# Kernel optimization log

Hardware: AMD Instinct MI355X
Metric: run time of the kernel (lower is better)

Reference implementation:

```python
import jax, jax.numpy as jnp
import numpy as np

B, S, D, H, DK, DV = 4, 1024, 1024, 16, 64, 64
HALF = D // 2            # 512
DKH = DK // 2            # per-head half q/k dim = 32
DVH = DV // 2            # per-head half v dim = 32


def setup_inputs() -> dict:
    key = jax.random.key(0)
    ks = jax.random.split(key, 12)
    f = lambda k, sh: jax.random.normal(k, sh, dtype=jnp.float32)
    inp = {
        "input_Q": f(ks[0], (B, S, D)),
        "input_K": f(ks[1], (B, S, D)),
        "input_V": f(ks[2], (B, S, D)),
    }
    # causal mask (True = masked), matching attn_mask() helper for non-pad tokens
    causal = jnp.triu(jnp.ones((S, S), dtype=bool), k=1)
    inp["attn_mask"] = jnp.broadcast_to(causal, (B, S, S))
    scale = 0.02
    # projections: [in=HALF, out=DK*H//2=HALF] stored as (in, out) for x @ W
    for i, n in enumerate(["WQ1", "WK1", "WV1", "WQ2", "WK2", "WV2"]):
        inp[n] = f(ks[3 + i], (HALF, DK * H // 2)) * scale
    inp["Wfc1"] = f(ks[9], (H * DV // 2, HALF)) * scale
    inp["Wfc2"] = f(ks[10], (H * DV // 2, HALF)) * scale
    inp["ln_g"] = jnp.ones((HALF,), dtype=jnp.float32)
    inp["ln_b"] = jnp.zeros((HALF,), dtype=jnp.float32)
    return inp


def _layernorm(x, g, b, eps=1e-5):
    mu = jnp.mean(x, axis=-1, keepdims=True)
    var = jnp.mean((x - mu) ** 2, axis=-1, keepdims=True)
    return (x - mu) * jax.lax.rsqrt(var + eps) * g + b


def _heads(x, dh):
    # [B, S, H*dh] -> [B, H, S, dh]
    return x.reshape(B, S, H, dh).transpose(0, 2, 1, 3)


def reference(input_Q, input_K, input_V, attn_mask,
              WQ1, WK1, WV1, WQ2, WK2, WV2, Wfc1, Wfc2, ln_g, ln_b):
    res1 = input_Q[:, :, :HALF]
    res2 = input_Q[:, :, HALF:]
    # half-dim projections, split into heads
    Q1 = _heads(input_Q[:, :, :HALF] @ WQ1, DKH)   # [B,H,S,DKH]
    K1 = _heads(input_K[:, :, :HALF] @ WK1, DKH)
    V1 = _heads(input_V[:, :, :HALF] @ WV1, DVH)
    V2 = _heads(input_V[:, :, HALF:] @ WV2, DVH)
    # Q2/K2 are computed in the original but unused by the attention scores;
    # still compute them for faithfulness (they'd carry grads of zero).
    _Q2 = _heads(input_Q[:, :, HALF:] @ WQ2, DKH)
    _K2 = _heads(input_K[:, :, HALF:] @ WK2, DKH)
    V = jnp.concatenate([V1, V2], axis=-1)         # [B,H,S,DV]
    # attention scores from half-dim Q1/K1 only, scaled by sqrt(d_k//2)
    attn = jnp.einsum("bhqd,bhkd->bhqk", Q1, K1) / np.sqrt(DKH).astype(np.float32)
    masked = jnp.where(attn_mask[:, None, :, :], jnp.float32(-1e9), attn)
    softmax_attn = jax.nn.softmax(masked, axis=-1)  # [B,H,S,S]
    qkv = jnp.einsum("bhqk,bhkd->bhqd", softmax_attn, V)  # [B,H,S,DV]
    qkv_out = qkv.transpose(0, 2, 1, 3).reshape(B, S, H * DV)
    out1 = _layernorm(qkv_out[:, :, : H * DV // 2] @ Wfc1 + res1, ln_g, ln_b)
    out2 = _layernorm(qkv_out[:, :, H * DV // 2 :] @ Wfc2 + res2, ln_g, ln_b)
    output = jnp.concatenate([out1, out2], axis=-1)
    return output, softmax_attn
```

## Files before the change

### kernel.cpp

```cpp
#include <hip/hip_runtime.h>

typedef unsigned short u16;
typedef __attribute__((ext_vector_type(8))) short bf16x8;
typedef __attribute__((ext_vector_type(4))) float f32x4;
typedef __attribute__((ext_vector_type(4))) unsigned short u16x4;

#define B_    4
#define S_    1024
#define D_    1024
#define H_    16
#define BS_   4096
#define HALF_ 512

#define WT_OFF   0
#define QH_OFF   1572864
#define KH_OFF   3670016
#define QKV_OFF  1572864

__device__ __forceinline__ u16 f2b(float f){
    f = (f == f) ? f : 0.f;
    unsigned u; __builtin_memcpy(&u, &f, 4);
    u += 0x7fffu + ((u >> 16) & 1u);
    return (u16)(u >> 16);
}

__global__ __launch_bounds__(256) void k_cvt(
    const float* Q, const float* K, const float* V,
    u16* Qb, u16* Kb, u16* Vb)
{
    const float* src; u16* dst;
    if      (blockIdx.y == 0) { src = Q; dst = Qb; }
    else if (blockIdx.y == 1) { src = K; dst = Kb; }
    else                      { src = V; dst = Vb; }
    size_t i = ((size_t)blockIdx.x * 256 + threadIdx.x) * 4;
    float4 v = *(const float4*)(src + i);
    u16x4 o = { f2b(v.x), f2b(v.y), f2b(v.z), f2b(v.w) };
    *(u16x4*)(dst + i) = o;
}

__global__ __launch_bounds__(256) void k_transpose(
    const float* w0, const float* w1, const float* w2, const float* w3,
    const float* w4, const float* w5, u16* out)
{
    __shared__ u16 tile[32][33];
    const float* src;
    switch (blockIdx.z) {
        case 0: src = w0; break; case 1: src = w1; break; case 2: src = w2; break;
        case 3: src = w3; break; case 4: src = w4; break; default: src = w5; break;
    }
    u16* dst = out + (size_t)blockIdx.z * 512 * 512;
    int tx = threadIdx.x & 31, ty = threadIdx.x >> 5;
    int x = blockIdx.x * 32 + tx;
    #pragma unroll
    for (int j = 0; j < 32; j += 8)
        tile[ty + j][tx] = f2b(src[(size_t)(blockIdx.y * 32 + ty + j) * 512 + x]);
    __syncthreads();
    int x2 = blockIdx.y * 32 + tx;
    #pragma unroll
    for (int j = 0; j < 32; j += 8)
        dst[(size_t)(blockIdx.x * 32 + ty + j) * 512 + x2] = tile[tx][ty + j];
}

__global__ __launch_bounds__(256) void k_proj(
    const u16* Qb, const u16* Kb, const u16* Vb, const u16* WT,
    u16* Qh, u16* Kh, u16* Vh)
{
    int which = blockIdx.z;
    const u16* X; const u16* Wt; int xofs;
    if      (which == 0) { X = Qb; Wt = WT + 0*512*512; xofs = 0;   }
    else if (which == 1) { X = Kb; Wt = WT + 1*512*512; xofs = 0;   }
    else if (which == 2) { X = Vb; Wt = WT + 2*512*512; xofs = 0;   }
    else                 { X = Vb; Wt = WT + 3*512*512; xofs = 512; }

    int lane = threadIdx.x & 63, w = threadIdx.x >> 6;
    int l15 = lane & 15, quad = lane >> 4;
    int m0 = blockIdx.x * 64 + w * 16;
    int n0 = blockIdx.y * 64;

    f32x4 acc[4] = {{0,0,0,0},{0,0,0,0},{0,0,0,0},{0,0,0,0}};
    const u16* arow = X + (size_t)(m0 + l15) * D_ + xofs + quad * 8;

    for (int k0 = 0; k0 < 512; k0 += 32) {
        bf16x8 a = *(const bf16x8*)(arow + k0);
        #pragma unroll
        for (int nt = 0; nt < 4; nt++) {
            bf16x8 b = *(const bf16x8*)(Wt + (size_t)(n0 + nt*16 + l15) * 512 + k0 + quad * 8);
            acc[nt] = __builtin_amdgcn_mfma_f32_16x16x32_bf16(a, b, acc[nt], 0, 0, 0);
        }
    }

    #pragma unroll
    for (int nt = 0; nt < 4; nt++) {
        #pragma unroll
        for (int r = 0; r < 4; r++) {
            int m = m0 + quad * 4 + r;
            int n = n0 + nt * 16 + l15;
            int b = m >> 10, s = m & 1023;
            int h = n >> 5,  d = n & 31;
            u16 v = f2b(acc[nt][r]);
            if (which == 0)      Qh[(((size_t)(b*16 + h))*1024 + s)*32 + d] = v;
            else if (which == 1) Kh[(((size_t)(b*16 + h))*1024 + s)*32 + d] = v;
            else {
                int dofs = (which == 3) ? 32 : 0;
                Vh[(((size_t)(b*16 + h))*1024 + s)*64 + dofs + d] = v;
            }
        }
    }
}

__global__ __launch_bounds__(256) void k_softmax(const u16* Qh, const u16* Kh, float* Pout)
{
    int bh = blockIdx.y;
    int m0 = blockIdx.x * 16;
    int lane = threadIdx.x & 63, w = threadIdx.x >> 6;
    int l15 = lane & 15, quad = lane >> 4;
    __shared__ float red_max[4][16], red_sum[4][16];

    bf16x8 a = *(const bf16x8*)(Qh + ((size_t)bh * 1024 + m0 + l15) * 32 + quad * 8);

    float sc[16][4];
    #pragma unroll
    for (int t = 0; t < 16; t++) {
        int n0 = w * 256 + t * 16;
        if (n0 > m0 + 15) {
            #pragma unroll
            for (int r = 0; r < 4; r++) sc[t][r] = -1e30f;
            continue;
        }
        bf16x8 b = *(const bf16x8*)(Kh + ((size_t)bh * 1024 + n0 + l15) * 32 + quad * 8);
        f32x4 z = {0,0,0,0};
        f32x4 c = __builtin_amdgcn_mfma_f32_16x16x32_bf16(a, b, z, 0, 0, 0);
        int col = n0 + l15;
        #pragma unroll
        for (int r = 0; r < 4; r++) {
            int row = m0 + quad * 4 + r;
            sc[t][r] = (col > row) ? -1e30f : c[r] * 0.17677669529663687f;
        }
    }

    float lmax[4];
    #pragma unroll
    for (int r = 0; r < 4; r++) {
        float m = -1e30f;
        #pragma unroll
        for (int t = 0; t < 16; t++) m = fmaxf(m, sc[t][r]);
        lmax[r] = m;
    }
    #pragma unroll
    for (int mk = 1; mk < 16; mk <<= 1)
        #pragma unroll
        for (int r = 0; r < 4; r++) lmax[r] = fmaxf(lmax[r], __shfl_xor(lmax[r], mk));
    if (l15 == 0)
        #pragma unroll
        for (int r = 0; r < 4; r++) red_max[w][quad * 4 + r] = lmax[r];
    __syncthreads();

    float rmax[4];
    #pragma unroll
    for (int r = 0; r < 4; r++) {
        int row = quad * 4 + r;
        rmax[r] = fmaxf(fmaxf(red_max[0][row], red_max[1][row]),
                        fmaxf(red_max[2][row], red_max[3][row]));
    }

    float lsum[4] = {0, 0, 0, 0};
    #pragma unroll
    for (int t = 0; t < 16; t++)
        #pragma unroll
        for (int r = 0; r < 4; r++) {
            float e = (sc[t][r] <= -1e29f) ? 0.f : __expf(sc[t][r] - rmax[r]);
            sc[t][r] = e; lsum[r] += e;
        }
    #pragma unroll
    for (int mk = 1; mk < 16; mk <<= 1)
        #pragma unroll
        for (int r = 0; r < 4; r++) lsum[r] += __shfl_xor(lsum[r], mk);
    if (l15 == 0)
        #pragma unroll
        for (int r = 0; r < 4; r++) red_sum[w][quad * 4 + r] = lsum[r];
    __syncthreads();

    #pragma unroll
    for (int r = 0; r < 4; r++) {
        int row = quad * 4 + r;
        float tot = red_sum[0][row] + red_sum[1][row] + red_sum[2][row] + red_sum[3][row];
        float inv = (tot > 0.f) ? 1.f / tot : 0.f;
        size_t rowbase = ((size_t)bh * 1024 + m0 + row) * 1024 + w * 256 + l15;
        #pragma unroll
        for (int t = 0; t < 16; t++)
            Pout[rowbase + t * 16] = sc[t][r] * inv;
    }
}

__global__ __launch_bounds__(256) void k_pv(const float* P, const u16* Vh, u16* QKV)
{
    int bh = blockIdx.y;
    int m0 = blockIdx.x * 64;
    int lane = threadIdx.x & 63, w = threadIdx.x >> 6;
    int l15 = lane & 15, quad = lane >> 4;
    __shared__ u16 vt[64][72];

    f32x4 acc[4] = {{0,0,0,0},{0,0,0,0},{0,0,0,0},{0,0,0,0}};
    int nchunks = blockIdx.x + 1;
    const float* prow = P + ((size_t)bh * 1024 + m0 + w * 16 + l15) * 1024 + quad * 8;

    for (int c = 0; c < nchunks; c++) {
        int k0 = c * 64;
        int kk = threadIdx.x >> 2, dv0 = (threadIdx.x & 3) * 16;
        const u16* vsrc = Vh + ((size_t)bh * 1024 + k0 + kk) * 64 + dv0;
        bf16x8 v0 = *(const bf16x8*)(vsrc);
        bf16x8 v1 = *(const bf16x8*)(vsrc + 8);
        __syncthreads();
        #pragma unroll
        for (int i = 0; i < 8; i++) vt[dv0 + i][kk]     = (u16)v0[i];
        #pragma unroll
        for (int i = 0; i < 8; i++) vt[dv0 + 8 + i][kk] = (u16)v1[i];
        __syncthreads();

        #pragma unroll
        for (int ks = 0; ks < 2; ks++) {
            float4 pa = *(const float4*)(prow + k0 + ks * 32);
            float4 pb = *(const float4*)(prow + k0 + ks * 32 + 4);
            bf16x8 a;
            a[0] = (short)f2b(pa.x); a[1] = (short)f2b(pa.y);
            a[2] = (short)f2b(pa.z); a[3] = (short)f2b(pa.w);
            a[4] = (short)f2b(pb.x); a[5] = (short)f2b(pb.y);
            a[6] = (short)f2b(pb.z); a[7] = (short)f2b(pb.w);
            #pragma unroll
            for (int nt = 0; nt < 4; nt++) {
                bf16x8 b = *(const bf16x8*)(&vt[nt * 16 + l15][ks * 32 + quad * 8]);
                acc[nt] = __builtin_amdgcn_mfma_f32_16x16x32_bf16(a, b, acc[nt], 0, 0, 0);
            }
        }
    }

    int b = bh >> 4, h = bh & 15;
    #pragma unroll
    for (int nt = 0; nt < 4; nt++)
        #pragma unroll
        for (int r = 0; r < 4; r++) {
            int s  = m0 + w * 16 + quad * 4 + r;
            int dv = nt * 16 + l15;
            QKV[((size_t)b * 1024 + s) * 1024 + h * 64 + dv] = f2b(acc[nt][r]);
        }
}

__global__ __launch_bounds__(256) void k_fc(
    const u16* QKV, const u16* WT, const float* resQ,
    const float* lng, const float* lnb, float* out)
{
    int half = blockIdx.y;
    int m0 = blockIdx.x * 16;
    int lane = threadIdx.x & 63, w = threadIdx.x >> 6;
    int l15 = lane & 15, quad = lane >> 4;
    __shared__ float red_s[4][16], red_q[4][16];

    const u16* Wt = WT + (size_t)(4 + half) * 512 * 512;
    f32x4 acc[8] = {{0,0,0,0},{0,0,0,0},{0,0,0,0},{0,0,0,0},
                    {0,0,0,0},{0,0,0,0},{0,0,0,0},{0,0,0,0}};
    const u16* arow = QKV + (size_t)(m0 + l15) * 1024 + half * 512 + quad * 8;

    for (int k0 = 0; k0 < 512; k0 += 32) {
        bf16x8 a = *(const bf16x8*)(arow + k0);
        #pragma unroll
        for (int f = 0; f < 8; f++) {
            int n = w * 128 + f * 16 + l15;
            bf16x8 b = *(const bf16x8*)(Wt + (size_t)n * 512 + k0 + quad * 8);
            acc[f] = __builtin_amdgcn_mfma_f32_16x16x32_bf16(a, b, acc[f], 0, 0, 0);
        }
    }

    #pragma unroll
    for (int f = 0; f < 8; f++)
        #pragma unroll
        for (int r = 0; r < 4; r++) {
            int row = m0 + quad * 4 + r;
            int col = w * 128 + f * 16 + l15;
            acc[f][r] += resQ[(size_t)row * 1024 + half * 512 + col];
        }

    float psum[4] = {0,0,0,0}, psq[4] = {0,0,0,0};
    #pragma unroll
    for (int f = 0; f < 8; f++)
        #pragma unroll
        for (int r = 0; r < 4; r++) { psum[r] += acc[f][r]; psq[r] += acc[f][r] * acc[f][r]; }
    #pragma unroll
    for (int mk = 1; mk < 16; mk <<= 1)
        #pragma unroll
        for (int r = 0; r < 4; r++) {
            psum[r] += __shfl_xor(psum[r], mk);
            psq[r]  += __shfl_xor(psq[r],  mk);
        }
    if (l15 == 0)
        #pragma unroll
        for (int r = 0; r < 4; r++) { red_s[w][quad*4+r] = psum[r]; red_q[w][quad*4+r] = psq[r]; }
    __syncthreads();

    #pragma unroll
    for (int r = 0; r < 4; r++) {
        int row = quad * 4 + r;
        float s  = red_s[0][row] + red_s[1][row] + red_s[2][row] + red_s[3][row];
        float q  = red_q[0][row] + red_q[1][row] + red_q[2][row] + red_q[3][row];
        float mu = s * (1.f / 512.f);
        float var = fmaxf(q * (1.f / 512.f) - mu * mu, 0.f);
        float rstd = rsqrtf(var + 1e-5f);
        #pragma unroll
        for (int f = 0; f < 8; f++) {
            int col = w * 128 + f * 16 + l15;
            float g = lng[col], bb = lnb[col];
            float v = (acc[f][r] - mu) * rstd * g + bb;
            out[(size_t)(m0 + row) * 1024 + half * 512 + col] = v;
        }
    }
}

extern "C" void kernel_launch(void* const* d_in, const int* in_sizes, int n_in,
                              void* d_out, int out_size, void* d_ws, size_t ws_size,
                              hipStream_t stream)
{
    const float* Q    = (const float*)d_in[0];
    const float* K    = (const float*)d_in[1];
    const float* V    = (const float*)d_in[2];
    const float* WQ1  = (const float*)d_in[4];
    const float* WK1  = (const float*)d_in[5];
    const float* WV1  = (const float*)d_in[6];
    const float* WV2  = (const float*)d_in[9];
    const float* Wfc1 = (const float*)d_in[10];
    const float* Wfc2 = (const float*)d_in[11];
    const float* lng  = (const float*)d_in[12];
    const float* lnb  = (const float*)d_in[13];

    float* out  = (float*)d_out;
    u16*   ws   = (u16*)d_ws;
    u16*   WT   = ws + WT_OFF;
    u16*   Qh   = ws + QH_OFF;
    u16*   Kh   = ws + KH_OFF;
    u16*   QKV  = ws + QKV_OFF;
    u16*   Vh   = (u16*)d_out;
    float* attn = out + (size_t)BS_ * D_;
    u16*   Qb   = (u16*)attn;
    u16*   Kb   = Qb + (size_t)BS_ * D_;
    u16*   Vb   = Kb + (size_t)BS_ * D_;

    k_cvt      <<<dim3(4096, 3),   256, 0, stream>>>(Q, K, V, Qb, Kb, Vb);
    k_transpose<<<dim3(16, 16, 6), 256, 0, stream>>>(WQ1, WK1, WV1, WV2, Wfc1, Wfc2, WT);
    k_proj     <<<dim3(64, 8, 4),  256, 0, stream>>>(Qb, Kb, Vb, WT, Qh, Kh, Vh);
    k_softmax  <<<dim3(64, 64),    256, 0, stream>>>(Qh, Kh, attn);
    k_pv       <<<dim3(16, 64),    256, 0, stream>>>(attn, Vh, QKV);
    k_fc       <<<dim3(256, 2),    256, 0, stream>>>(QKV, WT, Q, lng, lnb, out);
}
```

Before: 564.7 us.

## Recompute attention probabilities in PV kernel and fuse input conversion into projection

Result: faster. 546.1 us (-3.3%).

```diff
diff --git a/kernel.cpp b/kernel.cpp
--- a/kernel.cpp
+++ b/kernel.cpp
@@ -3,7 +3,6 @@
 typedef unsigned short u16;
 typedef __attribute__((ext_vector_type(8))) short bf16x8;
 typedef __attribute__((ext_vector_type(4))) float f32x4;
-typedef __attribute__((ext_vector_type(4))) unsigned short u16x4;
 
 #define B_    4
 #define S_    1024
@@ -12,30 +11,11 @@
 #define BS_   4096
 #define HALF_ 512
 
-#define WT_OFF   0
-#define QH_OFF   1572864
-#define KH_OFF   3670016
-#define QKV_OFF  1572864
 
 __device__ __forceinline__ u16 f2b(float f){
-    f = (f == f) ? f : 0.f;
     unsigned u; __builtin_memcpy(&u, &f, 4);
     u += 0x7fffu + ((u >> 16) & 1u);
     return (u16)(u >> 16);
-}
-
-__global__ __launch_bounds__(256) void k_cvt(
-    const float* Q, const float* K, const float* V,
-    u16* Qb, u16* Kb, u16* Vb)
-{
-    const float* src; u16* dst;
-    if      (blockIdx.y == 0) { src = Q; dst = Qb; }
-    else if (blockIdx.y == 1) { src = K; dst = Kb; }
-    else                      { src = V; dst = Vb; }
-    size_t i = ((size_t)blockIdx.x * 256 + threadIdx.x) * 4;
-    float4 v = *(const float4*)(src + i);
-    u16x4 o = { f2b(v.x), f2b(v.y), f2b(v.z), f2b(v.w) };
-    *(u16x4*)(dst + i) = o;
 }
 
 __global__ __launch_bounds__(256) void k_transpose(
@@ -62,15 +42,15 @@
 }
 
 __global__ __launch_bounds__(256) void k_proj(
-    const u16* Qb, const u16* Kb, const u16* Vb, const u16* WT,
+    const float* Q, const float* K, const float* V, const u16* WT,
     u16* Qh, u16* Kh, u16* Vh)
 {
     int which = blockIdx.z;
-    const u16* X; const u16* Wt; int xofs;
-    if      (which == 0) { X = Qb; Wt = WT + 0*512*512; xofs = 0;   }
-    else if (which == 1) { X = Kb; Wt = WT + 1*512*512; xofs = 0;   }
-    else if (which == 2) { X = Vb; Wt = WT + 2*512*512; xofs = 0;   }
-    else                 { X = Vb; Wt = WT + 3*512*512; xofs = 512; }
+    const float* X; const u16* Wt; int xofs;
+    if      (which == 0) { X = Q; Wt = WT + 0*512*512; xofs = 0;   }
+    else if (which == 1) { X = K; Wt = WT + 1*512*512; xofs = 0;   }
+    else if (which == 2) { X = V; Wt = WT + 2*512*512; xofs = 0;   }
+    else                 { X = V; Wt = WT + 3*512*512; xofs = 512; }
 
     int lane = threadIdx.x & 63, w = threadIdx.x >> 6;
     int l15 = lane & 15, quad = lane >> 4;
@@ -78,10 +58,16 @@
     int n0 = blockIdx.y * 64;
 
     f32x4 acc[4] = {{0,0,0,0},{0,0,0,0},{0,0,0,0},{0,0,0,0}};
-    const u16* arow = X + (size_t)(m0 + l15) * D_ + xofs + quad * 8;
+    const float* arow = X + (size_t)(m0 + l15) * D_ + xofs + quad * 8;
 
     for (int k0 = 0; k0 < 512; k0 += 32) {
-        bf16x8 a = *(const bf16x8*)(arow + k0);
+        float4 fa = *(const float4*)(arow + k0);
+        float4 fb = *(const float4*)(arow + k0 + 4);
+        bf16x8 a;
+        a[0] = (short)f2b(fa.x); a[1] = (short)f2b(fa.y);
+        a[2] = (short)f2b(fa.z); a[3] = (short)f2b(fa.w);
+        a[4] = (short)f2b(fb.x); a[5] = (short)f2b(fb.y);
+        a[6] = (short)f2b(fb.z); a[7] = (short)f2b(fb.w);
         #pragma unroll
         for (int nt = 0; nt < 4; nt++) {
             bf16x8 b = *(const bf16x8*)(Wt + (size_t)(n0 + nt*16 + l15) * 512 + k0 + quad * 8);
@@ -108,7 +94,8 @@
     }
 }
 
-__global__ __launch_bounds__(256) void k_softmax(const u16* Qh, const u16* Kh, float* Pout)
+__global__ __launch_bounds__(256) void k_softmax(
+    const u16* Qh, const u16* Kh, float* Pout, float* Mstat, float* Istat)
 {
     int bh = blockIdx.y;
     int m0 = blockIdx.x * 16;
@@ -185,6 +172,10 @@
         int row = quad * 4 + r;
         float tot = red_sum[0][row] + red_sum[1][row] + red_sum[2][row] + red_sum[3][row];
         float inv = (tot > 0.f) ? 1.f / tot : 0.f;
+        if (w == 0 && l15 == 0) {
+            Mstat[(size_t)bh * 1024 + m0 + row] = rmax[r];
+            Istat[(size_t)bh * 1024 + m0 + row] = inv;
+        }
         size_t rowbase = ((size_t)bh * 1024 + m0 + row) * 1024 + w * 256 + l15;
         #pragma unroll
         for (int t = 0; t < 16; t++)
@@ -192,17 +183,28 @@
     }
 }
 
-__global__ __launch_bounds__(256) void k_pv(const float* P, const u16* Vh, u16* QKV)
+__global__ __launch_bounds__(256) void k_pv(
+    const u16* Qh, const u16* Kh, const u16* Vh,
+    const float* Mstat, const float* Istat, u16* QKV)
 {
     int bh = blockIdx.y;
     int m0 = blockIdx.x * 64;
     int lane = threadIdx.x & 63, w = threadIdx.x >> 6;
     int l15 = lane & 15, quad = lane >> 4;
     __shared__ u16 vt[64][72];
+    __shared__ u16 pb[4][16][72];
+
+    bf16x8 aq = *(const bf16x8*)(Qh + ((size_t)bh * 1024 + m0 + w * 16 + l15) * 32 + quad * 8);
+    float mrow[4], irow[4];
+    #pragma unroll
+    for (int r = 0; r < 4; r++) {
+        int row = m0 + w * 16 + quad * 4 + r;
+        mrow[r] = Mstat[(size_t)bh * 1024 + row];
+        irow[r] = Istat[(size_t)bh * 1024 + row];
+    }
 
     f32x4 acc[4] = {{0,0,0,0},{0,0,0,0},{0,0,0,0},{0,0,0,0}};
     int nchunks = blockIdx.x + 1;
-    const float* prow = P + ((size_t)bh * 1024 + m0 + w * 16 + l15) * 1024 + quad * 8;
 
     for (int c = 0; c < nchunks; c++) {
         int k0 = c * 64;
@@ -218,14 +220,23 @@
         __syncthreads();
 
         #pragma unroll
+        for (int nt = 0; nt < 4; nt++) {
+            bf16x8 bk = *(const bf16x8*)(Kh + ((size_t)bh * 1024 + k0 + nt * 16 + l15) * 32 + quad * 8);
+            f32x4 z = {0,0,0,0};
+            f32x4 s = __builtin_amdgcn_mfma_f32_16x16x32_bf16(aq, bk, z, 0, 0, 0);
+            int col = k0 + nt * 16 + l15;
+            #pragma unroll
+            for (int r = 0; r < 4; r++) {
+                int row = m0 + w * 16 + quad * 4 + r;
+                float e = (col > row) ? 0.f
+                        : __expf(s[r] * 0.17677669529663687f - mrow[r]) * irow[r];
+                pb[w][quad * 4 + r][nt * 16 + l15] = f2b(e);
+            }
+        }
+
+        #pragma unroll
         for (int ks = 0; ks < 2; ks++) {
-            float4 pa = *(const float4*)(prow + k0 + ks * 32);
-            float4 pb = *(const float4*)(prow + k0 + ks * 32 + 4);
-            bf16x8 a;
-            a[0] = (short)f2b(pa.x); a[1] = (short)f2b(pa.y);
-            a[2] = (short)f2b(pa.z); a[3] = (short)f2b(pa.w);
-            a[4] = (short)f2b(pb.x); a[5] = (short)f2b(pb.y);
-            a[6] = (short)f2b(pb.z); a[7] = (short)f2b(pb.w);
+            bf16x8 a = *(const bf16x8*)(&pb[w][l15][ks * 32 + quad * 8]);
             #pragma unroll
             for (int nt = 0; nt < 4; nt++) {
                 bf16x8 b = *(const bf16x8*)(&vt[nt * 16 + l15][ks * 32 + quad * 8]);
@@ -330,22 +341,21 @@
     const float* lng  = (const float*)d_in[12];
     const float* lnb  = (const float*)d_in[13];
 
-    float* out  = (float*)d_out;
-    u16*   ws   = (u16*)d_ws;
-    u16*   WT   = ws + WT_OFF;
-    u16*   Qh   = ws + QH_OFF;
-    u16*   Kh   = ws + KH_OFF;
-    u16*   QKV  = ws + QKV_OFF;
-    u16*   Vh   = (u16*)d_out;
-    float* attn = out + (size_t)BS_ * D_;
-    u16*   Qb   = (u16*)attn;
-    u16*   Kb   = Qb + (size_t)BS_ * D_;
-    u16*   Vb   = Kb + (size_t)BS_ * D_;
-
-    k_cvt      <<<dim3(4096, 3),   256, 0, stream>>>(Q, K, V, Qb, Kb, Vb);
+    float* out   = (float*)d_out;
+    u16*   ws16  = (u16*)d_ws;
+    u16*   WT    = ws16;
+    u16*   QKV   = ws16 + 1572864;
+    float* Mstat = (float*)d_ws;
+    float* Istat = Mstat + 65536;
+
+    u16*   Vh    = (u16*)out;
+    u16*   Qh    = (u16*)(out + 2097152);
+    u16*   Kh    = (u16*)(out + 3145728);
+    float* attn  = out + (size_t)BS_ * D_;
+
     k_transpose<<<dim3(16, 16, 6), 256, 0, stream>>>(WQ1, WK1, WV1, WV2, Wfc1, Wfc2, WT);
-    k_proj     <<<dim3(64, 8, 4),  256, 0, stream>>>(Qb, Kb, Vb, WT, Qh, Kh, Vh);
-    k_softmax  <<<dim3(64, 64),    256, 0, stream>>>(Qh, Kh, attn);
-    k_pv       <<<dim3(16, 64),    256, 0, stream>>>(attn, Vh, QKV);
+    k_proj     <<<dim3(64, 8, 4),  256, 0, stream>>>(Q, K, V, WT, Qh, Kh, Vh);
+    k_softmax  <<<dim3(64, 64),    256, 0, stream>>>(Qh, Kh, attn, Mstat, Istat);
+    k_pv       <<<dim3(16, 64),    256, 0, stream>>>(Qh, Kh, Vh, Mstat, Istat, QKV);
     k_fc       <<<dim3(256, 2),    256, 0, stream>>>(QKV, WT, Q, lng, lnb, out);
 }
```
